# Performance work log

Measured on AMD Instinct MI355X. Metric: run time of the kernel, lower is better.

Reference implementation:

```python
import jax, jax.numpy as jnp
import numpy as np

N_NODES = 60000
IN_CH = 128
HID = 32
ACT_DIM = 6
N_EDGES = 600000


def setup_inputs() -> dict:
    key = jax.random.key(0)
    ks = jax.random.split(key, 10)
    state = jax.random.normal(ks[0], (N_NODES, IN_CH), dtype=jnp.float32)
    edge_index = jax.random.randint(ks[1], (2, N_EDGES), 0, N_NODES, dtype=jnp.int64)
    s_g = 1.0 / np.sqrt(IN_CH)
    s_h = 1.0 / np.sqrt(HID)
    Wg = jax.random.uniform(ks[2], (IN_CH, IN_CH), jnp.float32, -s_g, s_g)
    bg = jax.random.uniform(ks[3], (IN_CH,), jnp.float32, -s_g, s_g)
    W1 = jax.random.uniform(ks[4], (IN_CH, HID), jnp.float32, -s_g, s_g)
    b1 = jax.random.uniform(ks[5], (HID,), jnp.float32, -s_g, s_g)
    W2 = jax.random.uniform(ks[6], (HID, HID), jnp.float32, -s_h, s_h)
    b2 = jax.random.uniform(ks[7], (HID,), jnp.float32, -s_h, s_h)
    W3 = jax.random.uniform(ks[8], (HID, 1), jnp.float32, -s_h, s_h)
    b3 = jax.random.uniform(ks[9], (1,), jnp.float32, -s_h, s_h)
    return {"state": state, "Wg": Wg, "bg": bg, "W1": W1, "b1": b1,
            "W2": W2, "b2": b2, "W3": W3, "b3": b3, "edge_index": edge_index}


def reference(state, Wg, bg, W1, b1, W2, b2, W3, b3, edge_index):
    N = state.shape[0]
    # GCNConv: add self-loops, symmetric degree normalization
    loop = jnp.arange(N, dtype=edge_index.dtype)
    src = jnp.concatenate([edge_index[0], loop])
    dst = jnp.concatenate([edge_index[1], loop])
    deg = jax.ops.segment_sum(jnp.ones_like(dst, dtype=state.dtype), dst, num_segments=N)
    dinv = jax.lax.rsqrt(deg)  # deg >= 1 thanks to self-loops
    norm = dinv[src] * dinv[dst]  # [E+N]
    h = state @ Wg  # [N, C]
    agg = jax.ops.segment_sum(h[src] * norm[:, None], dst, num_segments=N) + bg
    out = jax.nn.relu(agg)
    x = (out + state).reshape(-1, ACT_DIM, IN_CH)  # [B, 6, C]
    x = jax.nn.leaky_relu(x @ W1 + b1)
    x = jax.nn.leaky_relu(x @ W2 + b2)
    conc = jax.nn.softplus(x @ W3 + b3)[..., 0]  # [B, 6]
    # deterministic, mode==0
    action = conc / (conc.sum() + 1e-20)
    return action
```

## Files before the change

### kernel.cpp

```cpp
#include <hip/hip_runtime.h>
#include <hip/hip_bf16.h>
#include <math.h>

#define N_NODES 60000
#define IN_CH   128
#define HID     32
#define N_EDGES 600000
#define CAP     32

#define WS_CNT    0
#define WS_SUM    60000
#define WS_BUCKET 60008
#define WS_HS     2940032
#define WS_X      10620032

typedef float  v4f __attribute__((ext_vector_type(4)));
typedef short  v8s __attribute__((ext_vector_type(8)));

static __device__ inline short f2bf(float f) {
    __hip_bfloat16 h = __float2bfloat16(f);
    union { __hip_bfloat16 h; short s; } u; u.h = h; return u.s;
}
static __device__ inline float bf2f(short s) {
    return __uint_as_float(((unsigned int)(unsigned short)s) << 16);
}
static __device__ inline float bflo(unsigned int u) { return __uint_as_float(u << 16); }
static __device__ inline float bfhi(unsigned int u) { return __uint_as_float(u & 0xffff0000u); }
static __device__ inline int   rdl_i(int v, int l)   { return __builtin_amdgcn_readlane(v, l); }
static __device__ inline float rdl_f(float v, int l) {
    return __int_as_float(__builtin_amdgcn_readlane(__float_as_int(v), l));
}

__launch_bounds__(256)
__global__ void k_fat(const float* __restrict__ state, const float* __restrict__ Wg,
                      const int* __restrict__ eidx, int* __restrict__ cnt,
                      unsigned short* __restrict__ bucket, unsigned short* __restrict__ hs) {
    __shared__ __align__(16) short Bs[128 * 136];
    const int bid = blockIdx.x;
    const int r7 = bid % 7, q7 = bid / 7;
    const int t = threadIdx.x;

    if (r7 >= 2) {
        const int hb = q7 * 5 + (r7 - 2);
        const int i = hb * 256 + t;
        if (i < N_EDGES) {
            int s = eidx[i];
            int d = eidx[N_EDGES + i];
            int slot = atomicAdd(&cnt[d], 1);
            if (slot < CAP) bucket[d * CAP + slot] = (unsigned short)s;
        }
        return;
    }

    const int gb = q7 * 2 + r7;

    for (int idx = t; idx < 128 * 128; idx += 256) {
        int k = idx >> 7, n = idx & 127;
        Bs[n * 136 + k] = f2bf(Wg[idx]);
    }
    __syncthreads();

    const int w = t >> 6, lane = t & 63;
    const int quad = lane >> 4, m = lane & 15;
    const int rowBase = gb * 64;
    int arow = rowBase + w * 16 + m;
    if (arow > N_NODES - 1) arow = N_NODES - 1;

    v8s a[4];
    const float4* sp = (const float4*)(state + (size_t)arow * 128);
#pragma unroll
    for (int q = 0; q < 4; ++q) {
        float4 v0 = sp[q * 8 + quad * 2];
        float4 v1 = sp[q * 8 + quad * 2 + 1];
        v8s af;
        af[0] = f2bf(v0.x); af[1] = f2bf(v0.y); af[2] = f2bf(v0.z); af[3] = f2bf(v0.w);
        af[4] = f2bf(v1.x); af[5] = f2bf(v1.y); af[6] = f2bf(v1.z); af[7] = f2bf(v1.w);
        a[q] = af;
    }

    v4f acc[8];
#pragma unroll
    for (int tt = 0; tt < 8; ++tt) acc[tt] = (v4f)0.f;

#pragma unroll
    for (int tt = 0; tt < 8; ++tt) {
        const short* bp = &Bs[(tt * 16 + m) * 136];
#pragma unroll
        for (int q = 0; q < 4; ++q) {
            v8s b = *(const v8s*)(bp + q * 32 + quad * 8);
            acc[tt] = __builtin_amdgcn_mfma_f32_16x16x32_bf16(a[q], b, acc[tt], 0, 0, 0);
        }
    }

#pragma unroll
    for (int tt = 0; tt < 8; ++tt) {
#pragma unroll
        for (int r = 0; r < 4; ++r) {
            int rr = rowBase + w * 16 + quad * 4 + r;
            if (rr < N_NODES)
                hs[(size_t)rr * 128 + tt * 16 + m] = (unsigned short)f2bf(acc[tt][r]);
        }
    }
}

__launch_bounds__(256)
__global__ void k_gather(const unsigned short* __restrict__ hs, const float* __restrict__ state,
                         const int* __restrict__ cnt, const unsigned short* __restrict__ bucket,
                         const float* __restrict__ bg, unsigned int* __restrict__ xb) {
    const int wave = threadIdx.x >> 6, lane = threadIdx.x & 63;
    const int row = blockIdx.x * 4 + wave;
    if (row >= N_NODES) return;
    const int ci = cnt[row];
    const float dinv = rsqrtf((float)ci + 1.0f);
    const int nb = ci < CAP ? ci : CAP;

    int slot = 0; float dv = 0.f;
    if (lane < nb) {
        slot = (int)bucket[row * CAP + lane];
        dv = rsqrtf((float)cnt[slot] + 1.0f);
    }

    const unsigned int* hp = (const unsigned int*)hs;
    float ax, ay;
    {
        unsigned int u = hp[(unsigned)row * 64u + lane];
        ax = bflo(u) * dinv;
        ay = bfhi(u) * dinv;
    }
    int s = 0;
    for (; s + 8 <= nb; s += 8) {
        int   s0 = rdl_i(slot, s + 0), s1 = rdl_i(slot, s + 1);
        int   s2 = rdl_i(slot, s + 2), s3 = rdl_i(slot, s + 3);
        int   s4 = rdl_i(slot, s + 4), s5 = rdl_i(slot, s + 5);
        int   s6 = rdl_i(slot, s + 6), s7 = rdl_i(slot, s + 7);
        float d0 = rdl_f(dv, s + 0), d1 = rdl_f(dv, s + 1);
        float d2 = rdl_f(dv, s + 2), d3 = rdl_f(dv, s + 3);
        float d4 = rdl_f(dv, s + 4), d5 = rdl_f(dv, s + 5);
        float d6 = rdl_f(dv, s + 6), d7 = rdl_f(dv, s + 7);
        unsigned int u0 = hp[(unsigned)s0 * 64u + lane];
        unsigned int u1 = hp[(unsigned)s1 * 64u + lane];
        unsigned int u2 = hp[(unsigned)s2 * 64u + lane];
        unsigned int u3 = hp[(unsigned)s3 * 64u + lane];
        unsigned int u4 = hp[(unsigned)s4 * 64u + lane];
        unsigned int u5 = hp[(unsigned)s5 * 64u + lane];
        unsigned int u6 = hp[(unsigned)s6 * 64u + lane];
        unsigned int u7 = hp[(unsigned)s7 * 64u + lane];
        ax = fmaf(d0, bflo(u0), ax); ay = fmaf(d0, bfhi(u0), ay);
        ax = fmaf(d1, bflo(u1), ax); ay = fmaf(d1, bfhi(u1), ay);
        ax = fmaf(d2, bflo(u2), ax); ay = fmaf(d2, bfhi(u2), ay);
        ax = fmaf(d3, bflo(u3), ax); ay = fmaf(d3, bfhi(u3), ay);
        ax = fmaf(d4, bflo(u4), ax); ay = fmaf(d4, bfhi(u4), ay);
        ax = fmaf(d5, bflo(u5), ax); ay = fmaf(d5, bfhi(u5), ay);
        ax = fmaf(d6, bflo(u6), ax); ay = fmaf(d6, bfhi(u6), ay);
        ax = fmaf(d7, bflo(u7), ax); ay = fmaf(d7, bfhi(u7), ay);
    }
    for (; s + 4 <= nb; s += 4) {
        int   s0 = rdl_i(slot, s + 0), s1 = rdl_i(slot, s + 1);
        int   s2 = rdl_i(slot, s + 2), s3 = rdl_i(slot, s + 3);
        float d0 = rdl_f(dv, s + 0), d1 = rdl_f(dv, s + 1);
        float d2 = rdl_f(dv, s + 2), d3 = rdl_f(dv, s + 3);
        unsigned int u0 = hp[(unsigned)s0 * 64u + lane];
        unsigned int u1 = hp[(unsigned)s1 * 64u + lane];
        unsigned int u2 = hp[(unsigned)s2 * 64u + lane];
        unsigned int u3 = hp[(unsigned)s3 * 64u + lane];
        ax = fmaf(d0, bflo(u0), ax); ay = fmaf(d0, bfhi(u0), ay);
        ax = fmaf(d1, bflo(u1), ax); ay = fmaf(d1, bfhi(u1), ay);
        ax = fmaf(d2, bflo(u2), ax); ay = fmaf(d2, bfhi(u2), ay);
        ax = fmaf(d3, bflo(u3), ax); ay = fmaf(d3, bfhi(u3), ay);
    }
    for (; s < nb; ++s) {
        int   s0 = rdl_i(slot, s);
        float d0 = rdl_f(dv, s);
        unsigned int u = hp[(unsigned)s0 * 64u + lane];
        ax = fmaf(d0, bflo(u), ax);
        ay = fmaf(d0, bfhi(u), ay);
    }
    float2 bgv = ((const float2*)bg)[lane];
    float2 st  = ((const float2*)state)[(unsigned)row * 64u + lane];
    float ox = fmaxf(fmaf(dinv, ax, bgv.x), 0.f) + st.x;
    float oy = fmaxf(fmaf(dinv, ay, bgv.y), 0.f) + st.y;
    unsigned int pack = ((unsigned int)(unsigned short)f2bf(oy) << 16)
                      | ((unsigned int)(unsigned short)f2bf(ox));
    xb[(unsigned)row * 64u + lane] = pack;
}

__launch_bounds__(256)
__global__ void k_mlp(const unsigned int* __restrict__ xb,
                      const float* __restrict__ W1, const float* __restrict__ b1,
                      const float* __restrict__ W2, const float* __restrict__ b2,
                      const float* __restrict__ W3, const float* __restrict__ b3,
                      float* __restrict__ out, float* __restrict__ sum) {
    __shared__ __align__(16) short BsH[32 * 136];
    __shared__ __align__(16) short BsL[32 * 136];
    __shared__ float  zs[4][16 * 33];
    __shared__ float4 W2s[32 * 8];
    __shared__ float  b1s[32], b2s[32], W3s[32];
    __shared__ float  wred[4];
    const int t = threadIdx.x;

    for (int idx = t; idx < 128 * 32; idx += 256) {
        int k = idx >> 5, j = idx & 31;
        float f = W1[idx];
        short hi = f2bf(f);
        short lo = f2bf(f - bf2f(hi));
        BsH[j * 136 + k] = hi;
        BsL[j * 136 + k] = lo;
    }
    W2s[t] = ((const float4*)W2)[t];
    if (t < 32) { b1s[t] = b1[t]; b2s[t] = b2[t]; W3s[t] = W3[t]; }
    __syncthreads();

    const int wv = t >> 6, lane = t & 63;
    const int quad = lane >> 4, m = lane & 15;
    const int rbase = (blockIdx.x * 4 + wv) * 16;
    float wavesum = 0.f;

    if (rbase < N_NODES) {
        v8s a[4];
        const int4* xp = (const int4*)(xb + (size_t)(rbase + m) * 64);
#pragma unroll
        for (int q = 0; q < 4; ++q) a[q] = *(const v8s*)&xp[q * 4 + quad];

        v4f acc0 = (v4f)0.f, acc1 = (v4f)0.f;
#pragma unroll
        for (int q = 0; q < 4; ++q) {
            v8s bh0 = *(const v8s*)&BsH[m * 136 + q * 32 + quad * 8];
            v8s bh1 = *(const v8s*)&BsH[(16 + m) * 136 + q * 32 + quad * 8];
            acc0 = __builtin_amdgcn_mfma_f32_16x16x32_bf16(a[q], bh0, acc0, 0, 0, 0);
            acc1 = __builtin_amdgcn_mfma_f32_16x16x32_bf16(a[q], bh1, acc1, 0, 0, 0);
        }
#pragma unroll
        for (int q = 0; q < 4; ++q) {
            v8s bl0 = *(const v8s*)&BsL[m * 136 + q * 32 + quad * 8];
            v8s bl1 = *(const v8s*)&BsL[(16 + m) * 136 + q * 32 + quad * 8];
            acc0 = __builtin_amdgcn_mfma_f32_16x16x32_bf16(a[q], bl0, acc0, 0, 0, 0);
            acc1 = __builtin_amdgcn_mfma_f32_16x16x32_bf16(a[q], bl1, acc1, 0, 0, 0);
        }

        float bj0 = b1s[m], bj1 = b1s[16 + m];
#pragma unroll
        for (int r = 0; r < 4; ++r) {
            float h0 = acc0[r] + bj0; h0 = h0 > 0.f ? h0 : 0.01f * h0;
            float h1 = acc1[r] + bj1; h1 = h1 > 0.f ? h1 : 0.01f * h1;
            zs[wv][(quad * 4 + r) * 33 + m]      = h0;
            zs[wv][(quad * 4 + r) * 33 + 16 + m] = h1;
        }
        asm volatile("s_waitcnt lgkmcnt(0)" ::: "memory");

        float h2[8];
#pragma unroll
        for (int j = 0; j < 8; ++j) h2[j] = b2s[quad * 8 + j];
        const float* zrow = &zs[wv][m * 33];
#pragma unroll
        for (int k = 0; k < 32; ++k) {
            float zk = zrow[k];
            float4 wA = W2s[k * 8 + quad * 2];
            float4 wB = W2s[k * 8 + quad * 2 + 1];
            h2[0] = fmaf(zk, wA.x, h2[0]); h2[1] = fmaf(zk, wA.y, h2[1]);
            h2[2] = fmaf(zk, wA.z, h2[2]); h2[3] = fmaf(zk, wA.w, h2[3]);
            h2[4] = fmaf(zk, wB.x, h2[4]); h2[5] = fmaf(zk, wB.y, h2[5]);
            h2[6] = fmaf(zk, wB.z, h2[6]); h2[7] = fmaf(zk, wB.w, h2[7]);
        }
        float a3p = 0.f;
#pragma unroll
        for (int j = 0; j < 8; ++j) {
            float z2 = h2[j] > 0.f ? h2[j] : 0.01f * h2[j];
            a3p = fmaf(z2, W3s[quad * 8 + j], a3p);
        }
        a3p += __shfl_xor(a3p, 16, 64);
        a3p += __shfl_xor(a3p, 32, 64);
        float a3 = a3p + b3[0];
        float sp = fmaxf(a3, 0.f) + log1pf(expf(-fabsf(a3)));
        if (quad == 0) out[rbase + m] = sp;
        float p = (quad == 0) ? sp : 0.f;
#pragma unroll
        for (int off = 32; off >= 1; off >>= 1) p += __shfl_xor(p, off, 64);
        wavesum = p;
    }
    if (lane == 0) wred[wv] = wavesum;
    __syncthreads();
    if (t == 0) atomicAdd(sum, (wred[0] + wred[1]) + (wred[2] + wred[3]));
}

__global__ void k_norm(const float* __restrict__ sum, float* __restrict__ out) {
    int i = blockIdx.x * blockDim.x + threadIdx.x;
    if (i < N_NODES / 4) {
        float inv = 1.0f / (*sum + 1e-20f);
        float4* o4 = (float4*)out;
        float4 v = o4[i];
        v.x *= inv; v.y *= inv; v.z *= inv; v.w *= inv;
        o4[i] = v;
    }
}

extern "C" void kernel_launch(void* const* d_in, const int* in_sizes, int n_in,
                              void* d_out, int out_size, void* d_ws, size_t ws_size,
                              hipStream_t stream) {
    const float* state = (const float*)d_in[0];
    const float* Wg    = (const float*)d_in[1];
    const float* bg    = (const float*)d_in[2];
    const float* W1    = (const float*)d_in[3];
    const float* b1    = (const float*)d_in[4];
    const float* W2    = (const float*)d_in[5];
    const float* b2    = (const float*)d_in[6];
    const float* W3    = (const float*)d_in[7];
    const float* b3    = (const float*)d_in[8];
    const int*   eidx  = (const int*)d_in[9];
    float* out = (float*)d_out;

    int*   wi = (int*)d_ws;
    float* wf = (float*)d_ws;
    int*   cnt    = wi + WS_CNT;
    float* sum    = wf + WS_SUM;
    unsigned short* bucket = (unsigned short*)(wi + WS_BUCKET);
    unsigned short* hs = (unsigned short*)(wf + WS_HS);
    unsigned int*   xb = (unsigned int*)(wf + WS_X);

    hipMemsetAsync(cnt, 0, 60001 * sizeof(int), stream);

    k_fat<<<3282, 256, 0, stream>>>(state, Wg, eidx, cnt, bucket, hs);
    k_gather<<<(N_NODES + 3) / 4, 256, 0, stream>>>(hs, state, cnt, bucket, bg, xb);
    k_mlp<<<938, 256, 0, stream>>>(xb, W1, b1, W2, b2, W3, b3, out, sum);
    k_norm<<<(N_NODES / 4 + 255) / 256, 256, 0, stream>>>(sum, out);
}
```

Before: 170.8 us.

## Process two rows per wave in gather and fold normalization into MLP last block

The gather kernel now gives each wave two destination rows, using lanes 0-31 for one row's neighbour slots and 32-63 for the other's. It issues eight independent row loads per iteration to raise memory-level parallelism and halve the block count. The separate normalization kernel is removed: the MLP kernel takes a ticket counter, and the last block to finish rescales the whole output by the global sum, saving one launch. The trade-offs are that the last block does a serial 60000-element pass, the paired rows iterate to the larger of their two neighbour counts, and a memset-cleared ticket counter is added.

Result: slower. 237.5 us (+39.0%).

```diff
diff --git a/kernel.cpp b/kernel.cpp
--- a/kernel.cpp
+++ b/kernel.cpp
@@ -10,6 +10,7 @@
 
 #define WS_CNT    0
 #define WS_SUM    60000
+#define WS_TICK   60001
 #define WS_BUCKET 60008
 #define WS_HS     2940032
 #define WS_X      10620032
@@ -108,80 +109,72 @@
                          const int* __restrict__ cnt, const unsigned short* __restrict__ bucket,
                          const float* __restrict__ bg, unsigned int* __restrict__ xb) {
     const int wave = threadIdx.x >> 6, lane = threadIdx.x & 63;
-    const int row = blockIdx.x * 4 + wave;
-    if (row >= N_NODES) return;
-    const int ci = cnt[row];
-    const float dinv = rsqrtf((float)ci + 1.0f);
-    const int nb = ci < CAP ? ci : CAP;
-
-    int slot = 0; float dv = 0.f;
-    if (lane < nb) {
-        slot = (int)bucket[row * CAP + lane];
-        dv = rsqrtf((float)cnt[slot] + 1.0f);
-    }
-
+    const int row0 = blockIdx.x * 8 + wave * 2;
+    if (row0 >= N_NODES) return;
+    const int row1 = row0 + 1;
+
+    const int ci0 = cnt[row0];
+    const int ci1 = cnt[row1];
+    int sl = (int)bucket[(size_t)row0 * CAP + lane];
     const unsigned int* hp = (const unsigned int*)hs;
-    float ax, ay;
-    {
-        unsigned int u = hp[(unsigned)row * 64u + lane];
-        ax = bflo(u) * dinv;
-        ay = bfhi(u) * dinv;
-    }
-    int s = 0;
-    for (; s + 8 <= nb; s += 8) {
-        int   s0 = rdl_i(slot, s + 0), s1 = rdl_i(slot, s + 1);
-        int   s2 = rdl_i(slot, s + 2), s3 = rdl_i(slot, s + 3);
-        int   s4 = rdl_i(slot, s + 4), s5 = rdl_i(slot, s + 5);
-        int   s6 = rdl_i(slot, s + 6), s7 = rdl_i(slot, s + 7);
-        float d0 = rdl_f(dv, s + 0), d1 = rdl_f(dv, s + 1);
-        float d2 = rdl_f(dv, s + 2), d3 = rdl_f(dv, s + 3);
-        float d4 = rdl_f(dv, s + 4), d5 = rdl_f(dv, s + 5);
-        float d6 = rdl_f(dv, s + 6), d7 = rdl_f(dv, s + 7);
-        unsigned int u0 = hp[(unsigned)s0 * 64u + lane];
-        unsigned int u1 = hp[(unsigned)s1 * 64u + lane];
-        unsigned int u2 = hp[(unsigned)s2 * 64u + lane];
-        unsigned int u3 = hp[(unsigned)s3 * 64u + lane];
-        unsigned int u4 = hp[(unsigned)s4 * 64u + lane];
-        unsigned int u5 = hp[(unsigned)s5 * 64u + lane];
-        unsigned int u6 = hp[(unsigned)s6 * 64u + lane];
-        unsigned int u7 = hp[(unsigned)s7 * 64u + lane];
-        ax = fmaf(d0, bflo(u0), ax); ay = fmaf(d0, bfhi(u0), ay);
-        ax = fmaf(d1, bflo(u1), ax); ay = fmaf(d1, bfhi(u1), ay);
-        ax = fmaf(d2, bflo(u2), ax); ay = fmaf(d2, bfhi(u2), ay);
-        ax = fmaf(d3, bflo(u3), ax); ay = fmaf(d3, bfhi(u3), ay);
-        ax = fmaf(d4, bflo(u4), ax); ay = fmaf(d4, bfhi(u4), ay);
-        ax = fmaf(d5, bflo(u5), ax); ay = fmaf(d5, bfhi(u5), ay);
-        ax = fmaf(d6, bflo(u6), ax); ay = fmaf(d6, bfhi(u6), ay);
-        ax = fmaf(d7, bflo(u7), ax); ay = fmaf(d7, bfhi(u7), ay);
-    }
-    for (; s + 4 <= nb; s += 4) {
-        int   s0 = rdl_i(slot, s + 0), s1 = rdl_i(slot, s + 1);
-        int   s2 = rdl_i(slot, s + 2), s3 = rdl_i(slot, s + 3);
-        float d0 = rdl_f(dv, s + 0), d1 = rdl_f(dv, s + 1);
-        float d2 = rdl_f(dv, s + 2), d3 = rdl_f(dv, s + 3);
-        unsigned int u0 = hp[(unsigned)s0 * 64u + lane];
-        unsigned int u1 = hp[(unsigned)s1 * 64u + lane];
-        unsigned int u2 = hp[(unsigned)s2 * 64u + lane];
-        unsigned int u3 = hp[(unsigned)s3 * 64u + lane];
-        ax = fmaf(d0, bflo(u0), ax); ay = fmaf(d0, bfhi(u0), ay);
-        ax = fmaf(d1, bflo(u1), ax); ay = fmaf(d1, bfhi(u1), ay);
-        ax = fmaf(d2, bflo(u2), ax); ay = fmaf(d2, bfhi(u2), ay);
-        ax = fmaf(d3, bflo(u3), ax); ay = fmaf(d3, bfhi(u3), ay);
-    }
-    for (; s < nb; ++s) {
-        int   s0 = rdl_i(slot, s);
-        float d0 = rdl_f(dv, s);
-        unsigned int u = hp[(unsigned)s0 * 64u + lane];
-        ax = fmaf(d0, bflo(u), ax);
-        ay = fmaf(d0, bfhi(u), ay);
-    }
+    unsigned int us0 = hp[(unsigned)row0 * 64u + lane];
+    unsigned int us1 = hp[(unsigned)row1 * 64u + lane];
     float2 bgv = ((const float2*)bg)[lane];
-    float2 st  = ((const float2*)state)[(unsigned)row * 64u + lane];
-    float ox = fmaxf(fmaf(dinv, ax, bgv.x), 0.f) + st.x;
-    float oy = fmaxf(fmaf(dinv, ay, bgv.y), 0.f) + st.y;
-    unsigned int pack = ((unsigned int)(unsigned short)f2bf(oy) << 16)
-                      | ((unsigned int)(unsigned short)f2bf(ox));
-    xb[(unsigned)row * 64u + lane] = pack;
+    float2 st0 = ((const float2*)state)[(unsigned)row0 * 64u + lane];
+    float2 st1 = ((const float2*)state)[(unsigned)row1 * 64u + lane];
+
+    const float dinv0 = rsqrtf((float)ci0 + 1.0f);
+    const float dinv1 = rsqrtf((float)ci1 + 1.0f);
+    const int nb0 = ci0 < CAP ? ci0 : CAP;
+    const int nb1 = ci1 < CAP ? ci1 : CAP;
+
+    const bool valid = (lane < 32) ? (lane < nb0) : ((lane - 32) < nb1);
+    int slot = 0; float dvv = 0.f;
+    if (valid) {
+        slot = sl;
+        dvv = rsqrtf((float)cnt[slot] + 1.0f);
+    }
+
+    float ax0 = bflo(us0) * dinv0, ay0 = bfhi(us0) * dinv0;
+    float ax1 = bflo(us1) * dinv1, ay1 = bfhi(us1) * dinv1;
+
+    const int nmax = nb0 > nb1 ? nb0 : nb1;
+    for (int s = 0; s < nmax; s += 4) {
+        int   a0 = rdl_i(slot, s + 0), a1 = rdl_i(slot, s + 1);
+        int   a2 = rdl_i(slot, s + 2), a3 = rdl_i(slot, s + 3);
+        int   b0 = rdl_i(slot, 32 + s + 0), b1 = rdl_i(slot, 32 + s + 1);
+        int   b2 = rdl_i(slot, 32 + s + 2), b3 = rdl_i(slot, 32 + s + 3);
+        float e0 = rdl_f(dvv, s + 0), e1 = rdl_f(dvv, s + 1);
+        float e2 = rdl_f(dvv, s + 2), e3 = rdl_f(dvv, s + 3);
+        float f0 = rdl_f(dvv, 32 + s + 0), f1 = rdl_f(dvv, 32 + s + 1);
+        float f2 = rdl_f(dvv, 32 + s + 2), f3 = rdl_f(dvv, 32 + s + 3);
+        unsigned int ua0 = hp[(unsigned)a0 * 64u + lane];
+        unsigned int ua1 = hp[(unsigned)a1 * 64u + lane];
+        unsigned int ua2 = hp[(unsigned)a2 * 64u + lane];
+        unsigned int ua3 = hp[(unsigned)a3 * 64u + lane];
+        unsigned int ub0 = hp[(unsigned)b0 * 64u + lane];
+        unsigned int ub1 = hp[(unsigned)b1 * 64u + lane];
+        unsigned int ub2 = hp[(unsigned)b2 * 64u + lane];
+        unsigned int ub3 = hp[(unsigned)b3 * 64u + lane];
+        ax0 = fmaf(e0, bflo(ua0), ax0); ay0 = fmaf(e0, bfhi(ua0), ay0);
+        ax0 = fmaf(e1, bflo(ua1), ax0); ay0 = fmaf(e1, bfhi(ua1), ay0);
+        ax0 = fmaf(e2, bflo(ua2), ax0); ay0 = fmaf(e2, bfhi(ua2), ay0);
+        ax0 = fmaf(e3, bflo(ua3), ax0); ay0 = fmaf(e3, bfhi(ua3), ay0);
+        ax1 = fmaf(f0, bflo(ub0), ax1); ay1 = fmaf(f0, bfhi(ub0), ay1);
+        ax1 = fmaf(f1, bflo(ub1), ax1); ay1 = fmaf(f1, bfhi(ub1), ay1);
+        ax1 = fmaf(f2, bflo(ub2), ax1); ay1 = fmaf(f2, bfhi(ub2), ay1);
+        ax1 = fmaf(f3, bflo(ub3), ax1); ay1 = fmaf(f3, bfhi(ub3), ay1);
+    }
+    float ox0 = fmaxf(fmaf(dinv0, ax0, bgv.x), 0.f) + st0.x;
+    float oy0 = fmaxf(fmaf(dinv0, ay0, bgv.y), 0.f) + st0.y;
+    float ox1 = fmaxf(fmaf(dinv1, ax1, bgv.x), 0.f) + st1.x;
+    float oy1 = fmaxf(fmaf(dinv1, ay1, bgv.y), 0.f) + st1.y;
+    unsigned int p0 = ((unsigned int)(unsigned short)f2bf(oy0) << 16)
+                    | ((unsigned int)(unsigned short)f2bf(ox0));
+    unsigned int p1 = ((unsigned int)(unsigned short)f2bf(oy1) << 16)
+                    | ((unsigned int)(unsigned short)f2bf(ox1));
+    xb[(unsigned)row0 * 64u + lane] = p0;
+    xb[(unsigned)row1 * 64u + lane] = p1;
 }
 
 __launch_bounds__(256)
@@ -189,13 +182,14 @@
                       const float* __restrict__ W1, const float* __restrict__ b1,
                       const float* __restrict__ W2, const float* __restrict__ b2,
                       const float* __restrict__ W3, const float* __restrict__ b3,
-                      float* __restrict__ out, float* __restrict__ sum) {
+                      float* __restrict__ out, float* __restrict__ sum, int* __restrict__ tick) {
     __shared__ __align__(16) short BsH[32 * 136];
     __shared__ __align__(16) short BsL[32 * 136];
     __shared__ float  zs[4][16 * 33];
     __shared__ float4 W2s[32 * 8];
     __shared__ float  b1s[32], b2s[32], W3s[32];
     __shared__ float  wred[4];
+    __shared__ int    lastblk;
     const int t = threadIdx.x;
 
     for (int idx = t; idx < 128 * 32; idx += 256) {
@@ -237,20 +231,21 @@
             acc1 = __builtin_amdgcn_mfma_f32_16x16x32_bf16(a[q], bl1, acc1, 0, 0, 0);
         }
 
+        float* zsw = zs[wv];
         float bj0 = b1s[m], bj1 = b1s[16 + m];
 #pragma unroll
         for (int r = 0; r < 4; ++r) {
             float h0 = acc0[r] + bj0; h0 = h0 > 0.f ? h0 : 0.01f * h0;
             float h1 = acc1[r] + bj1; h1 = h1 > 0.f ? h1 : 0.01f * h1;
-            zs[wv][(quad * 4 + r) * 33 + m]      = h0;
-            zs[wv][(quad * 4 + r) * 33 + 16 + m] = h1;
+            zsw[(quad * 4 + r) * 33 + m]      = h0;
+            zsw[(quad * 4 + r) * 33 + 16 + m] = h1;
         }
         asm volatile("s_waitcnt lgkmcnt(0)" ::: "memory");
 
         float h2[8];
 #pragma unroll
         for (int j = 0; j < 8; ++j) h2[j] = b2s[quad * 8 + j];
-        const float* zrow = &zs[wv][m * 33];
+        const float* zrow = &zsw[m * 33];
 #pragma unroll
         for (int k = 0; k < 32; ++k) {
             float zk = zrow[k];
@@ -279,17 +274,21 @@
     }
     if (lane == 0) wred[wv] = wavesum;
     __syncthreads();
-    if (t == 0) atomicAdd(sum, (wred[0] + wred[1]) + (wred[2] + wred[3]));
-}
-
-__global__ void k_norm(const float* __restrict__ sum, float* __restrict__ out) {
-    int i = blockIdx.x * blockDim.x + threadIdx.x;
-    if (i < N_NODES / 4) {
-        float inv = 1.0f / (*sum + 1e-20f);
-        float4* o4 = (float4*)out;
-        float4 v = o4[i];
-        v.x *= inv; v.y *= inv; v.z *= inv; v.w *= inv;
-        o4[i] = v;
+    if (t == 0) {
+        atomicAdd(sum, (wred[0] + wred[1]) + (wred[2] + wred[3]));
+        __threadfence();
+        int ticket = atomicAdd(tick, 1);
+        lastblk = (ticket == (int)gridDim.x - 1);
+    }
+    __syncthreads();
+    if (lastblk) {
+        __threadfence();
+        float sv = __hip_atomic_load(sum, __ATOMIC_RELAXED, __HIP_MEMORY_SCOPE_AGENT);
+        float inv = 1.0f / (sv + 1e-20f);
+        for (int i = t; i < N_NODES; i += 256) {
+            float v = __hip_atomic_load(&out[i], __ATOMIC_RELAXED, __HIP_MEMORY_SCOPE_AGENT);
+            out[i] = v * inv;
+        }
     }
 }
 
@@ -312,14 +311,14 @@
     float* wf = (float*)d_ws;
     int*   cnt    = wi + WS_CNT;
     float* sum    = wf + WS_SUM;
+    int*   tick   = wi + WS_TICK;
     unsigned short* bucket = (unsigned short*)(wi + WS_BUCKET);
     unsigned short* hs = (unsigned short*)(wf + WS_HS);
     unsigned int*   xb = (unsigned int*)(wf + WS_X);
 
-    hipMemsetAsync(cnt, 0, 60001 * sizeof(int), stream);
+    hipMemsetAsync(cnt, 0, 60002 * sizeof(int), stream);
 
     k_fat<<<3282, 256, 0, stream>>>(state, Wg, eidx, cnt, bucket, hs);
-    k_gather<<<(N_NODES + 3) / 4, 256, 0, stream>>>(hs, state, cnt, bucket, bg, xb);
-    k_mlp<<<938, 256, 0, stream>>>(xb, W1, b1, W2, b2, W3, b3, out, sum);
-    k_norm<<<(N_NODES / 4 + 255) / 256, 256, 0, stream>>>(sum, out);
-}
+    k_gather<<<(N_NODES + 7) / 8, 256, 0, stream>>>(hs, state, cnt, bucket, bg, xb);
+    k_mlp<<<938, 256, 0, stream>>>(xb, W1, b1, W2, b2, W3, b3, out, sum, tick);
+}
```
